# Kernel optimization log

Measured on AMD Instinct MI355X. Metric: run time of the kernel, lower is better.

Reference implementation:

```python
import jax, jax.numpy as jnp
import numpy as np

WS = 8        # window size
NH = 3        # num heads (head_dim = 192/3 = 64)
EPS = 1e-5    # BatchNorm eps


def conv1x1(x, w, b):
    # x: [B,C,H,W], w: [O,C], b: [O]  (1x1 conv == per-pixel matmul)
    return jnp.einsum('bchw,oc->bohw', x, w) + b[None, :, None, None]


def bn(x, gamma, beta, mean, var):
    # eval-mode BatchNorm2d
    scale = gamma / jnp.sqrt(var + EPS)
    return x * scale[None, :, None, None] + (beta - mean * scale)[None, :, None, None]


def window_partition_nchw(x, ws):
    # Faithful replication of the torch view/permute sequence (incl. its
    # channel/width interleaving inside each window).
    B, C, H, W = x.shape
    pad_h = (ws - H % ws) % ws
    pad_w = (ws - W % ws) % ws
    if pad_h or pad_w:
        x = jnp.pad(x, ((0, 0), (0, 0), (0, pad_h), (0, pad_w)))
    Hp, Wp = H + pad_h, W + pad_w
    x = x.reshape(B, C, Hp // ws, ws, Wp)
    windows = jnp.transpose(x, (0, 2, 4, 1, 3)).reshape(-1, C, ws, ws)
    return windows, (Hp, Wp)


def window_unpartition_nchw(windows, ws, pad_hw, hw):
    Hp, Wp = pad_hw
    H, W = hw
    B = windows.shape[0] // (Hp * Wp // ws // ws)
    C = windows.shape[1]
    x = windows.reshape(B, Hp // ws, Wp // ws, C, ws * ws)
    x = jnp.transpose(x, (0, 3, 1, 2, 4)).reshape(B, C, Hp, Wp)
    return x[:, :, :H, :W]


def attention(x, qkv_w, qkv_b, proj_w, proj_b):
    # x: [Nwin, C, ws, ws]
    B, C, H, W = x.shape
    qkv = conv1x1(x, qkv_w, qkv_b)              # [B, 3*D, H, W]
    D = qkv.shape[1] // 3
    hd = D // NH
    qkv = qkv.reshape(B, 3, NH, hd, H * W)
    q, k, v = qkv[:, 0], qkv[:, 1], qkv[:, 2]   # [B, NH, hd, N]
    scale = hd ** -0.5
    attn = jnp.einsum('bhdn,bhdm->bhnm', q, k) * scale   # [B,NH,Nq,Nk]
    attn = jax.nn.softmax(attn, axis=-1)
    o = jnp.einsum('bhdm,bhnm->bhdn', v, attn).reshape(B, D, H, W)
    return conv1x1(o, proj_w, proj_b)


def setup_inputs() -> dict:
    key = jax.random.key(0)
    ks = jax.random.split(key, 16)
    B, C, H, W = 16, 192, 128, 128
    D = C            # dim_out == dim
    HID = 4 * D      # mlp_ratio = 4
    s = 0.02
    inp = {
        'x':           jax.random.normal(ks[0], (B, C, H, W), jnp.float32),
        'bn1_gamma':   jnp.ones((C,), jnp.float32),
        'bn1_beta':    jnp.zeros((C,), jnp.float32),
        'bn1_mean':    jax.random.normal(ks[1], (C,), jnp.float32) * 0.1,
        'bn1_var':     jax.random.uniform(ks[2], (C,), jnp.float32, 0.5, 1.5),
        'qkv_w':       jax.random.normal(ks[3], (3 * D, C), jnp.float32) * s,
        'qkv_b':       jnp.zeros((3 * D,), jnp.float32),
        'attn_proj_w': jax.random.normal(ks[4], (D, D), jnp.float32) * s,
        'attn_proj_b': jnp.zeros((D,), jnp.float32),
        'bn2_gamma':   jnp.ones((D,), jnp.float32),
        'bn2_beta':    jnp.zeros((D,), jnp.float32),
        'bn2_mean':    jax.random.normal(ks[5], (D,), jnp.float32) * 0.1,
        'bn2_var':     jax.random.uniform(ks[6], (D,), jnp.float32, 0.5, 1.5),
        'mlp_w1':      jax.random.normal(ks[7], (HID, D), jnp.float32) * s,
        'mlp_b1':      jnp.zeros((HID,), jnp.float32),
        'mlp_w2':      jax.random.normal(ks[8], (D, HID), jnp.float32) * s,
        'mlp_b2':      jnp.zeros((D,), jnp.float32),
    }
    return inp


def reference(x, bn1_gamma, bn1_beta, bn1_mean, bn1_var,
              qkv_w, qkv_b, attn_proj_w, attn_proj_b,
              bn2_gamma, bn2_beta, bn2_mean, bn2_var,
              mlp_w1, mlp_b1, mlp_w2, mlp_b2):
    shortcut = x
    h = bn(x, bn1_gamma, bn1_beta, bn1_mean, bn1_var)
    win, pad_hw = window_partition_nchw(h, WS)
    a = attention(win, qkv_w, qkv_b, attn_proj_w, attn_proj_b)
    a = window_unpartition_nchw(a, WS, pad_hw, (x.shape[2], x.shape[3]))
    x2 = shortcut + a                       # residual 1 (drop_path = identity)
    m = bn(x2, bn2_gamma, bn2_beta, bn2_mean, bn2_var)
    m = conv1x1(m, mlp_w1, mlp_b1)
    m = jax.nn.gelu(m, approximate=False)   # torch nn.GELU default (exact erf)
    m = conv1x1(m, mlp_w2, mlp_b2)
    return x2 + m                           # residual 2
```

## Files before the change

### kernel.cpp

```cpp
#include <hip/hip_runtime.h>
#include <hip/hip_bf16.h>
#include <math.h>

#define DI __device__ __forceinline__

typedef short bf16x8 __attribute__((ext_vector_type(8)));
typedef float f32x4 __attribute__((ext_vector_type(4)));
typedef unsigned short u16;

DI u16 f2bf(float f){
  unsigned u = __float_as_uint(f);
  unsigned r = (u + 0x7FFFu + ((u>>16)&1u)) >> 16;
  return (u16)r;
}
DI float bf2f(u16 h){ return __uint_as_float(((unsigned)h)<<16); }
DI unsigned pack2(float a, float b){ return (unsigned)f2bf(a) | ((unsigned)f2bf(b)<<16); }
DI float gelu_exact(float v){ return 0.5f*v*(1.0f + erff(v*0.70710678118654752f)); }

DI void gload_lds16(const void* g, const void* l){
  __builtin_amdgcn_global_load_lds((const __attribute__((address_space(1))) void*)g,
                                   (__attribute__((address_space(3))) void*)(void*)l, 16, 0, 0);
}

__global__ __launch_bounds__(256) void k0_prep(const float* __restrict__ qkvw,
    const float* __restrict__ pw, const float* __restrict__ w1, const float* __restrict__ w2,
    u16* __restrict__ wq, u16* __restrict__ wp, u16* __restrict__ w1b, u16* __restrict__ w2b){
  int i = blockIdx.x*256 + threadIdx.x;
  if (i < 122880){
    int r = i/192;
    u16 v = 0;
    if (r < 576) v = f2bf(qkvw[i]);
    wq[i] = v;
  } else if (i < 172032){
    int j = i-122880; int r = j/192;
    u16 v = 0;
    if (r < 192) v = f2bf(pw[j]);
    wp[j] = v;
  } else if (i < 319488){
    int j = i-172032; w1b[j] = f2bf(w1[j]);
  } else if (i < 516096){
    int j = i-319488; int r = j/768;
    u16 v = 0;
    if (r < 192) v = f2bf(w2[j]);
    w2b[j] = v;
  }
}

__global__ __launch_bounds__(512) void k1_part(const float* __restrict__ x,
    const float* __restrict__ g1, const float* __restrict__ b1,
    const float* __restrict__ m1, const float* __restrict__ v1,
    u16* __restrict__ win_t){
  __shared__ u16 so[4*64*200];
  int tid = threadIdx.x;
  int bx = blockIdx.x;
  int wg = bx & 3, hb = (bx>>2)&15, b = bx>>6;
#pragma unroll
  for (int i=0;i<24;i++){
    int lin = i*512 + tid;
    int w4 = lin & 7;
    int rowid = lin >> 3;
    int c = rowid >> 3, jj = rowid & 7;
    float sc = g1[c]*rsqrtf(v1[c]+1e-5f);
    float sh = b1[c] - m1[c]*sc;
    float4 xv = *(const float4*)(x + (((size_t)(b*192 + c)*128 + hb*8 + jj)*128 + wg*32 + w4*4));
    int cg = c>>3, ci = c&7;
    int t = ci*8 + jj;
    float vv[4] = {xv.x, xv.y, xv.z, xv.w};
#pragma unroll
    for (int k=0;k<4;k++){
      int w = w4*4 + k;
      int wig = w>>3, q = w&7;
      so[(wig*64 + t)*200 + q*24 + cg] = f2bf(vv[k]*sc + sh);
    }
  }
  __syncthreads();
  int rowi = tid>>1, half = tid&1;
  size_t tok0 = ((size_t)((b*16+hb)*16 + wg*4))*64;
  u16* dst = win_t + (tok0 + rowi)*192 + half*96;
  const u16* src = so + rowi*200 + half*96;
#pragma unroll
  for (int ch=0; ch<12; ch++)
    *(uint4*)(dst + ch*8) = *(const uint4*)(src + ch*8);
}

template<int EPI>
__global__ __launch_bounds__(256) void gemm_k(
    const u16* __restrict__ A, const u16* __restrict__ B,
    const float* __restrict__ bias, const float* __restrict__ x2,
    u16* __restrict__ outA, u16* __restrict__ outB, float* __restrict__ outF,
    int K, int Mtiles, int Mvalid, size_t Nstr)
{
  __shared__ u16 As[128*32];
  __shared__ u16 Bs[128*32];
  int tid = threadIdx.x;
  int wid = tid>>6, lane = tid&63;
  int lm = lane&15, g = lane>>4;
  int bx = blockIdx.x;
  int mt = bx % Mtiles;
  size_t n0 = (size_t)(bx / Mtiles) * 128;
  int m0 = mt*128;
  int wm = wid>>1, wn = wid&1;

  f32x4 acc[4][4];
#pragma unroll
  for (int i=0;i<4;i++)
#pragma unroll
    for (int j=0;j<4;j++) acc[i][j] = (f32x4){0.f,0.f,0.f,0.f};

  int nK = K >> 5;
  for (int kt=0; kt<nK; kt++){
    int kk = kt<<5;
#pragma unroll
    for (int s=0;s<2;s++){
      int seg = s*256 + tid;
      int row = seg>>2, ch = seg&3;
      int chs = ch ^ (row&3);
      gload_lds16(A + (size_t)(m0+row)*K + kk + chs*8, (const char*)As + (s*256 + wid*64)*16);
      gload_lds16(B + (n0+(size_t)row)*K + kk + chs*8, (const char*)Bs + (s*256 + wid*64)*16);
    }
    asm volatile("s_waitcnt vmcnt(0)" ::: "memory");
    __syncthreads();
    bf16x8 af[4], bfr[4];
#pragma unroll
    for (int i=0;i<4;i++){
      int row = wm*64 + i*16 + lm;
      af[i]  = *(const bf16x8*)&As[row*32 + ((g ^ (row&3))<<3)];
      int rb  = wn*64 + i*16 + lm;
      bfr[i] = *(const bf16x8*)&Bs[rb*32 + ((g ^ (rb&3))<<3)];
    }
#pragma unroll
    for (int i=0;i<4;i++)
#pragma unroll
      for (int j=0;j<4;j++)
        acc[i][j] = __builtin_amdgcn_mfma_f32_16x16x32_bf16(af[i], bfr[j], acc[i][j], 0,0,0);
    __syncthreads();
  }

  int baseM = m0 + wm*64;
  size_t nbase = n0 + wn*64;

  if (EPI == 0){
    if (m0 < 384){
#pragma unroll
      for (int i=0;i<4;i++){
        int mcol = baseM + i*16 + 4*g;
        float b0=bias[mcol], b1_=bias[mcol+1], b2_=bias[mcol+2], b3_=bias[mcol+3];
#pragma unroll
        for (int j=0;j<4;j++){
          size_t tok = nbase + j*16 + lm;
          f32x4 v = acc[i][j];
          uint2 w; w.x = pack2(v[0]+b0, v[1]+b1_); w.y = pack2(v[2]+b2_, v[3]+b3_);
          *(uint2*)(outA + tok*384 + mcol) = w;
        }
      }
    } else {
#pragma unroll
      for (int i=0;i<4;i++)
#pragma unroll
        for (int j=0;j<4;j++){
          f32x4 v = acc[i][j];
#pragma unroll
          for (int r=0;r<4;r++){
            int m = baseM + i*16 + 4*g + r;
            if (m < Mvalid){
              size_t tok = nbase + j*16 + lm;
              outB[(size_t)(m-384)*Nstr + tok] = f2bf(v[r] + bias[m]);
            }
          }
        }
    }
  }
  if (EPI == 1){
#pragma unroll
    for (int i=0;i<4;i++)
#pragma unroll
      for (int j=0;j<4;j++){
        f32x4 v = acc[i][j];
#pragma unroll
        for (int r=0;r<4;r++){
          int m = baseM + i*16 + 4*g + r;
          if (m < Mvalid){
            size_t tok = nbase + j*16 + lm;
            outB[(size_t)m*Nstr + tok] = f2bf(v[r] + bias[m]);
          }
        }
      }
  }
  if (EPI == 2){
#pragma unroll
    for (int i=0;i<4;i++){
      int mcol = baseM + i*16 + 4*g;
      float b0=bias[mcol], b1_=bias[mcol+1], b2_=bias[mcol+2], b3_=bias[mcol+3];
#pragma unroll
      for (int j=0;j<4;j++){
        size_t tok = nbase + j*16 + lm;
        f32x4 v = acc[i][j];
        uint2 w;
        w.x = pack2(gelu_exact(v[0]+b0), gelu_exact(v[1]+b1_));
        w.y = pack2(gelu_exact(v[2]+b2_), gelu_exact(v[3]+b3_));
        *(uint2*)(outA + tok*768 + mcol) = w;
      }
    }
  }
  if (EPI == 3){
#pragma unroll
    for (int i=0;i<4;i++)
#pragma unroll
      for (int j=0;j<4;j++){
        f32x4 v = acc[i][j];
#pragma unroll
        for (int r=0;r<4;r++){
          int m = baseM + i*16 + 4*g + r;
          if (m < Mvalid){
            size_t nn = nbase + j*16 + lm;
            size_t bimg = nn>>14; size_t p = nn & 16383;
            size_t off = (bimg*192 + m)*16384 + p;
            outF[off] = v[r] + bias[m] + x2[off];
          }
        }
      }
  }
}

__global__ __launch_bounds__(192) void k3_attn(const u16* __restrict__ qkt,
    const u16* __restrict__ vb, u16* __restrict__ ot, size_t Nstr){
  __shared__ u16 lds[3*3*4096];
  int tid = threadIdx.x;
  int hd = tid>>6;
  int lane = tid&63;
  int lm = lane&15, g = lane>>4;
  size_t win = blockIdx.x;
  u16* Kt = lds + hd*3*4096;
  u16* Vt = Kt + 4096;
  u16* QP = Vt + 4096;
  size_t tokb = win*64;

#pragma unroll
  for (int it=0; it<8; it++){
    int seg = it*64 + lane;
    int row = seg>>3, c16 = seg&7;
    int cs = (c16 ^ (row&7))*8;
    gload_lds16(qkt + (tokb+row)*384 + 192 + hd*64 + cs, (const char*)Kt + it*1024);
    gload_lds16(qkt + (tokb+row)*384 +       hd*64 + cs, (const char*)QP + it*1024);
    gload_lds16(vb + (size_t)(hd*64+row)*Nstr + tokb + cs, (const char*)Vt + it*1024);
  }
  asm volatile("s_waitcnt vmcnt(0)" ::: "memory");

  bf16x8 ak[4][2];
#pragma unroll
  for (int mt2=0; mt2<4; mt2++)
#pragma unroll
    for (int kd=0; kd<2; kd++){
      int row = mt2*16 + lm;
      ak[mt2][kd] = *(const bf16x8*)&Kt[row*64 + (((kd*4+g) ^ (row&7))<<3)];
    }

  float rinv[4];
#pragma unroll
  for (int nt=0; nt<4; nt++){
    int rowq = nt*16 + lm;
    bf16x8 bq0 = *(const bf16x8*)&QP[rowq*64 + (((0+g) ^ (rowq&7))<<3)];
    bf16x8 bq1 = *(const bf16x8*)&QP[rowq*64 + (((4+g) ^ (rowq&7))<<3)];
    f32x4 sa[4];
#pragma unroll
    for (int mt2=0; mt2<4; mt2++){
      f32x4 z = (f32x4){0.f,0.f,0.f,0.f};
      z = __builtin_amdgcn_mfma_f32_16x16x32_bf16(ak[mt2][0], bq0, z, 0,0,0);
      z = __builtin_amdgcn_mfma_f32_16x16x32_bf16(ak[mt2][1], bq1, z, 0,0,0);
      sa[mt2] = z;
    }
    float mx = -1e30f;
#pragma unroll
    for (int mt2=0; mt2<4; mt2++)
#pragma unroll
      for (int r=0;r<4;r++) mx = fmaxf(mx, sa[mt2][r]);
    mx = fmaxf(mx, __shfl_xor(mx, 16));
    mx = fmaxf(mx, __shfl_xor(mx, 32));
    float sum = 0.f;
    float e[4][4];
#pragma unroll
    for (int mt2=0; mt2<4; mt2++)
#pragma unroll
      for (int r=0;r<4;r++){ float t = __expf(0.125f*(sa[mt2][r]-mx)); e[mt2][r] = t; sum += t; }
    sum += __shfl_xor(sum, 16);
    sum += __shfl_xor(sum, 32);
    rinv[nt] = 1.0f / sum;
    int n = nt*16 + lm;
#pragma unroll
    for (int mt2=0; mt2<4; mt2++)
#pragma unroll
      for (int pr=0; pr<2; pr++){
        int m = mt2*16 + 4*g + pr*2;
        *(unsigned*)&QP[n*64 + (((m>>3) ^ (n&7))<<3) + (m&7)] = pack2(e[mt2][pr*2], e[mt2][pr*2+1]);
      }
  }

  f32x4 oa[4][4];
#pragma unroll
  for (int i=0;i<4;i++)
#pragma unroll
    for (int j=0;j<4;j++) oa[i][j] = (f32x4){0.f,0.f,0.f,0.f};
  bf16x8 av[4][2];
#pragma unroll
  for (int dt=0; dt<4; dt++)
#pragma unroll
    for (int km=0; km<2; km++){
      int row = dt*16 + lm;
      av[dt][km] = *(const bf16x8*)&Vt[row*64 + (((km*4+g) ^ (row&7))<<3)];
    }
#pragma unroll
  for (int nt=0; nt<4; nt++){
    int rowp = nt*16 + lm;
    bf16x8 bp0 = *(const bf16x8*)&QP[rowp*64 + (((0+g) ^ (rowp&7))<<3)];
    bf16x8 bp1 = *(const bf16x8*)&QP[rowp*64 + (((4+g) ^ (rowp&7))<<3)];
#pragma unroll
    for (int dt=0; dt<4; dt++){
      oa[dt][nt] = __builtin_amdgcn_mfma_f32_16x16x32_bf16(av[dt][0], bp0, oa[dt][nt], 0,0,0);
      oa[dt][nt] = __builtin_amdgcn_mfma_f32_16x16x32_bf16(av[dt][1], bp1, oa[dt][nt], 0,0,0);
    }
  }
#pragma unroll
  for (int nt=0; nt<4; nt++){
    size_t tok = tokb + nt*16 + lm;
#pragma unroll
    for (int dt=0; dt<4; dt++){
      f32x4 v = oa[dt][nt];
      uint2 w;
      w.x = pack2(v[0]*rinv[nt], v[1]*rinv[nt]);
      w.y = pack2(v[2]*rinv[nt], v[3]*rinv[nt]);
      *(uint2*)(ot + tok*192 + hd*64 + dt*16 + 4*g) = w;
    }
  }
}

__global__ __launch_bounds__(512) void k5_unpart(const u16* __restrict__ aw,
    const float* __restrict__ x, float* __restrict__ x2, size_t Nstr){
  __shared__ u16 abuf[192*288];
  int tid = threadIdx.x;
  int bx = blockIdx.x;
  int wg = bx&3, hb = (bx>>2)&15, b = bx>>6;
  size_t tok0 = ((size_t)((b*16+hb)*16 + wg*4))*64;
#pragma unroll
  for (int i=0;i<12;i++){
    int idx = i*512 + tid;
    int cp = idx>>5, l32 = idx&31;
    uint4 v = *(const uint4*)(aw + (size_t)cp*Nstr + tok0 + l32*8);
    int q = cp/24, cg = cp - q*24;
    int ci = l32&7, wig = l32>>3;
    int c = cg*8 + ci;
    const u16* pv = (const u16*)&v;
#pragma unroll
    for (int k=0;k<8;k++)
      abuf[c*288 + k*36 + wig*8 + q] = pv[k];
  }
  __syncthreads();
#pragma unroll
  for (int i=0;i<24;i++){
    int lin = i*512 + tid;
    int w4 = lin&7, rowid = lin>>3;
    int c = rowid>>3, jj = rowid&7;
    size_t xoff = ((size_t)(b*192 + c)*128 + hb*8 + jj)*128 + wg*32 + w4*4;
    float4 xv = *(const float4*)(x + xoff);
    float vv[4] = {xv.x, xv.y, xv.z, xv.w};
    float4 o;
    o.x = vv[0] + bf2f(abuf[c*288 + jj*36 + w4*4 + 0]);
    o.y = vv[1] + bf2f(abuf[c*288 + jj*36 + w4*4 + 1]);
    o.z = vv[2] + bf2f(abuf[c*288 + jj*36 + w4*4 + 2]);
    o.w = vv[3] + bf2f(abuf[c*288 + jj*36 + w4*4 + 3]);
    *(float4*)(x2 + xoff) = o;
  }
}

__global__ __launch_bounds__(256) void k5b_t(const float* __restrict__ x2,
    const float* __restrict__ g2, const float* __restrict__ be2,
    const float* __restrict__ m2, const float* __restrict__ v2,
    u16* __restrict__ h2t){
  __shared__ u16 t[64*260];
  int tid = threadIdx.x;
  int bx = blockIdx.x;
  int b = bx/192; int rem = bx - b*192; int cb = rem>>6; int pb = rem&63;
#pragma unroll
  for (int i=0;i<16;i++){
    int idx = i*256 + tid;
    int cr = idx>>6, p4 = idx&63;
    int c = cb*64 + cr;
    float sc = g2[c]*rsqrtf(v2[c]+1e-5f);
    float sh = be2[c] - m2[c]*sc;
    float4 v = *(const float4*)(x2 + ((size_t)(b*192+c)*16384 + pb*256 + p4*4));
    uint2 w; w.x = pack2(v.x*sc+sh, v.y*sc+sh); w.y = pack2(v.z*sc+sh, v.w*sc+sh);
    *(uint2*)&t[cr*260 + p4*4] = w;
  }
  __syncthreads();
  size_t tokg = (size_t)b*16384 + pb*256 + tid;
  u16* dst = h2t + tokg*192 + cb*64;
#pragma unroll
  for (int cc=0; cc<8; cc++){
    u16 tmp[8];
#pragma unroll
    for (int k=0;k<8;k++) tmp[k] = t[(cc*8+k)*260 + tid];
    *(uint4*)(dst + cc*8) = *(const uint4*)tmp;
  }
}

extern "C" void kernel_launch(void* const* d_in, const int* in_sizes, int n_in,
                              void* d_out, int out_size, void* d_ws, size_t ws_size,
                              hipStream_t stream){
  const float* x   = (const float*)d_in[0];
  const float* g1  = (const float*)d_in[1];
  const float* be1 = (const float*)d_in[2];
  const float* mu1 = (const float*)d_in[3];
  const float* va1 = (const float*)d_in[4];
  const float* qkvw= (const float*)d_in[5];
  const float* qkvb= (const float*)d_in[6];
  const float* pw  = (const float*)d_in[7];
  const float* pb  = (const float*)d_in[8];
  const float* g2  = (const float*)d_in[9];
  const float* be2 = (const float*)d_in[10];
  const float* mu2 = (const float*)d_in[11];
  const float* va2 = (const float*)d_in[12];
  const float* w1  = (const float*)d_in[13];
  const float* b1  = (const float*)d_in[14];
  const float* w2  = (const float*)d_in[15];
  const float* b2  = (const float*)d_in[16];
  float* out = (float*)d_out;
  char* ws = (char*)d_ws;

  const size_t MB = 1048576;
  u16*  wint = (u16*) (ws + 0*MB);
  u16*  vbuf = (u16*) (ws + 24*MB);
  u16*  o_t  = (u16*) (ws + 48*MB);
  u16*  awin = (u16*) (ws + 72*MB);
  u16*  gt   = (u16*) (ws + 0*MB);
  u16*  qkt  = (u16*) (ws + 96*MB);
  u16*  h2t  = (u16*) (ws + 96*MB);
  u16*  wq   = (u16*) (ws + 144*MB);
  u16*  wp   = wq  + 640*192;
  u16*  w1b  = wp  + 256*192;
  u16*  w2b  = w1b + 768*192;
  const size_t needed = 144*MB + 1032192;
  if (ws_size < needed) return;

  const size_t SLICE_TOK = 65536;
  const size_t SLICE_ELT = SLICE_TOK * 192;

  k0_prep<<<2016,256,0,stream>>>(qkvw, pw, w1, w2, wq, wp, w1b, w2b);

  for (int s=0; s<4; s++){
    const float* xs = x   + (size_t)s*SLICE_ELT;
    float*      x2s = out + (size_t)s*SLICE_ELT;
    k1_part<<<256,512,0,stream>>>(xs, g1, be1, mu1, va1, wint);
    gemm_k<0><<<512*5,256,0,stream>>>(wq, wint, qkvb, nullptr,
                                      qkt, vbuf, nullptr, 192, 5, 576, SLICE_TOK);
    k3_attn<<<1024,192,0,stream>>>(qkt, vbuf, o_t, SLICE_TOK);
    gemm_k<1><<<512*2,256,0,stream>>>(wp, o_t, pb, nullptr,
                                      nullptr, awin, nullptr, 192, 2, 192, SLICE_TOK);
    k5_unpart<<<256,512,0,stream>>>(awin, xs, x2s, SLICE_TOK);
  }

  for (int s=0; s<4; s++){
    float* x2s = out + (size_t)s*SLICE_ELT;
    k5b_t<<<768,256,0,stream>>>(x2s, g2, be2, mu2, va2, h2t);
    gemm_k<2><<<512*6,256,0,stream>>>(w1b, h2t, b1, nullptr,
                                      gt, nullptr, nullptr, 192, 6, 768, SLICE_TOK);
    gemm_k<3><<<512*2,256,0,stream>>>(w2b, gt, b2, x2s,
                                      nullptr, nullptr, x2s, 768, 2, 192, SLICE_TOK);
  }
}
```

Measured before the change: 1.618 ms.

## Process all tokens in one pass, fuse BN2 transpose into unpartition, remap GEMM blocks

Drops the four-way token slicing, so each stage runs once over all 262144 tokens with larger grids. A much larger workspace holds the full-size intermediates. The BN2 plus transpose kernel is folded into the unpartition kernel, which now writes both x2 and the bf16 token-major normalized activations through a swizzled LDS buffer, avoiding a re-read of x2. GEMM block IDs are remapped across 8 groups (likely meant to match XCD dispatch) to improve cache locality. The trade-offs are higher workspace memory and more register pressure in the fused kernel (48 packed values per thread).

```diff
diff --git a/kernel.cpp b/kernel.cpp
--- a/kernel.cpp
+++ b/kernel.cpp
@@ -95,9 +95,12 @@
   int tid = threadIdx.x;
   int wid = tid>>6, lane = tid&63;
   int lm = lane&15, g = lane>>4;
-  int bx = blockIdx.x;
-  int mt = bx % Mtiles;
-  size_t n0 = (size_t)(bx / Mtiles) * 128;
+  int nwg = gridDim.x;
+  int chunk = nwg >> 3;
+  int bid = blockIdx.x;
+  int wgid = (bid & 7) * chunk + (bid >> 3);
+  int mt = wgid % Mtiles;
+  size_t n0 = (size_t)(wgid / Mtiles) * 128;
   int m0 = mt*128;
   int wm = wid>>1, wn = wid&1;
 
@@ -334,7 +337,10 @@
 }
 
 __global__ __launch_bounds__(512) void k5_unpart(const u16* __restrict__ aw,
-    const float* __restrict__ x, float* __restrict__ x2, size_t Nstr){
+    const float* __restrict__ x,
+    const float* __restrict__ g2, const float* __restrict__ be2,
+    const float* __restrict__ m2, const float* __restrict__ v2,
+    float* __restrict__ x2, u16* __restrict__ h2t, size_t Nstr){
   __shared__ u16 abuf[192*288];
   int tid = threadIdx.x;
   int bx = blockIdx.x;
@@ -354,51 +360,48 @@
       abuf[c*288 + k*36 + wig*8 + q] = pv[k];
   }
   __syncthreads();
+  unsigned hreg[48];
 #pragma unroll
   for (int i=0;i<24;i++){
     int lin = i*512 + tid;
     int w4 = lin&7, rowid = lin>>3;
     int c = rowid>>3, jj = rowid&7;
+    float sc = g2[c]*rsqrtf(v2[c]+1e-5f);
+    float sh = be2[c] - m2[c]*sc;
     size_t xoff = ((size_t)(b*192 + c)*128 + hb*8 + jj)*128 + wg*32 + w4*4;
     float4 xv = *(const float4*)(x + xoff);
-    float vv[4] = {xv.x, xv.y, xv.z, xv.w};
     float4 o;
-    o.x = vv[0] + bf2f(abuf[c*288 + jj*36 + w4*4 + 0]);
-    o.y = vv[1] + bf2f(abuf[c*288 + jj*36 + w4*4 + 1]);
-    o.z = vv[2] + bf2f(abuf[c*288 + jj*36 + w4*4 + 2]);
-    o.w = vv[3] + bf2f(abuf[c*288 + jj*36 + w4*4 + 3]);
+    o.x = xv.x + bf2f(abuf[c*288 + jj*36 + w4*4 + 0]);
+    o.y = xv.y + bf2f(abuf[c*288 + jj*36 + w4*4 + 1]);
+    o.z = xv.z + bf2f(abuf[c*288 + jj*36 + w4*4 + 2]);
+    o.w = xv.w + bf2f(abuf[c*288 + jj*36 + w4*4 + 3]);
     *(float4*)(x2 + xoff) = o;
-  }
-}
-
-__global__ __launch_bounds__(256) void k5b_t(const float* __restrict__ x2,
-    const float* __restrict__ g2, const float* __restrict__ be2,
-    const float* __restrict__ m2, const float* __restrict__ v2,
-    u16* __restrict__ h2t){
-  __shared__ u16 t[64*260];
-  int tid = threadIdx.x;
-  int bx = blockIdx.x;
-  int b = bx/192; int rem = bx - b*192; int cb = rem>>6; int pb = rem&63;
-#pragma unroll
-  for (int i=0;i<16;i++){
-    int idx = i*256 + tid;
-    int cr = idx>>6, p4 = idx&63;
-    int c = cb*64 + cr;
-    float sc = g2[c]*rsqrtf(v2[c]+1e-5f);
-    float sh = be2[c] - m2[c]*sc;
-    float4 v = *(const float4*)(x2 + ((size_t)(b*192+c)*16384 + pb*256 + p4*4));
-    uint2 w; w.x = pack2(v.x*sc+sh, v.y*sc+sh); w.y = pack2(v.z*sc+sh, v.w*sc+sh);
-    *(uint2*)&t[cr*260 + p4*4] = w;
+    hreg[i*2]   = pack2(o.x*sc+sh, o.y*sc+sh);
+    hreg[i*2+1] = pack2(o.z*sc+sh, o.w*sc+sh);
   }
   __syncthreads();
-  size_t tokg = (size_t)b*16384 + pb*256 + tid;
-  u16* dst = h2t + tokg*192 + cb*64;
-#pragma unroll
-  for (int cc=0; cc<8; cc++){
-    u16 tmp[8];
-#pragma unroll
-    for (int k=0;k<8;k++) tmp[k] = t[(cc*8+k)*260 + tid];
-    *(uint4*)(dst + cc*8) = *(const uint4*)tmp;
+#pragma unroll
+  for (int i=0;i<24;i++){
+    int lin = i*512 + tid;
+    int w4 = lin&7, rowid = lin>>3;
+    int c = rowid>>3, jj = rowid&7;
+    const u16* hv = (const u16*)&hreg[i*2];
+#pragma unroll
+    for (int k=0;k<4;k++){
+      int lt = jj*32 + w4*4 + k;
+      abuf[lt*192 + (c ^ ((lt&7)<<3))] = hv[k];
+    }
+  }
+  __syncthreads();
+  int rowi = tid>>1, half = tid&1;
+  int jj2 = rowi>>5, w2 = rowi&31;
+  size_t tokg = (size_t)b*16384 + (size_t)(hb*8 + jj2)*128 + wg*32 + w2;
+  u16* dst = h2t + tokg*192;
+#pragma unroll
+  for (int ch=0; ch<12; ch++){
+    int cc = half*12 + ch;
+    uint4 v = *(const uint4*)&abuf[rowi*192 + (((cc*16) ^ ((rowi&7)<<4))>>1)];
+    *(uint4*)(dst + cc*8) = v;
   }
 }
 
@@ -427,42 +430,31 @@
 
   const size_t MB = 1048576;
   u16*  wint = (u16*) (ws + 0*MB);
-  u16*  vbuf = (u16*) (ws + 24*MB);
-  u16*  o_t  = (u16*) (ws + 48*MB);
-  u16*  awin = (u16*) (ws + 72*MB);
-  u16*  gt   = (u16*) (ws + 0*MB);
+  u16*  o_t  = (u16*) (ws + 0*MB);
+  u16*  h2t  = (u16*) (ws + 0*MB);
   u16*  qkt  = (u16*) (ws + 96*MB);
-  u16*  h2t  = (u16*) (ws + 96*MB);
-  u16*  wq   = (u16*) (ws + 144*MB);
+  u16*  awin = (u16*) (ws + 96*MB);
+  u16*  gt   = (u16*) (ws + 96*MB);
+  u16*  vbuf = (u16*) (ws + 288*MB);
+  u16*  wq   = (u16*) (ws + 480*MB);
   u16*  wp   = wq  + 640*192;
   u16*  w1b  = wp  + 256*192;
   u16*  w2b  = w1b + 768*192;
-  const size_t needed = 144*MB + 1032192;
+  const size_t needed = 480*MB + 1032192;
   if (ws_size < needed) return;
 
-  const size_t SLICE_TOK = 65536;
-  const size_t SLICE_ELT = SLICE_TOK * 192;
+  const size_t NTOK = 262144;
 
   k0_prep<<<2016,256,0,stream>>>(qkvw, pw, w1, w2, wq, wp, w1b, w2b);
-
-  for (int s=0; s<4; s++){
-    const float* xs = x   + (size_t)s*SLICE_ELT;
-    float*      x2s = out + (size_t)s*SLICE_ELT;
-    k1_part<<<256,512,0,stream>>>(xs, g1, be1, mu1, va1, wint);
-    gemm_k<0><<<512*5,256,0,stream>>>(wq, wint, qkvb, nullptr,
-                                      qkt, vbuf, nullptr, 192, 5, 576, SLICE_TOK);
-    k3_attn<<<1024,192,0,stream>>>(qkt, vbuf, o_t, SLICE_TOK);
-    gemm_k<1><<<512*2,256,0,stream>>>(wp, o_t, pb, nullptr,
-                                      nullptr, awin, nullptr, 192, 2, 192, SLICE_TOK);
-    k5_unpart<<<256,512,0,stream>>>(awin, xs, x2s, SLICE_TOK);
-  }
-
-  for (int s=0; s<4; s++){
-    float* x2s = out + (size_t)s*SLICE_ELT;
-    k5b_t<<<768,256,0,stream>>>(x2s, g2, be2, mu2, va2, h2t);
-    gemm_k<2><<<512*6,256,0,stream>>>(w1b, h2t, b1, nullptr,
-                                      gt, nullptr, nullptr, 192, 6, 768, SLICE_TOK);
-    gemm_k<3><<<512*2,256,0,stream>>>(w2b, gt, b2, x2s,
-                                      nullptr, nullptr, x2s, 768, 2, 192, SLICE_TOK);
-  }
-}
+  k1_part<<<1024,512,0,stream>>>(x, g1, be1, mu1, va1, wint);
+  gemm_k<0><<<10240,256,0,stream>>>(wq, wint, qkvb, nullptr,
+                                    qkt, vbuf, nullptr, 192, 5, 576, NTOK);
+  k3_attn<<<4096,192,0,stream>>>(qkt, vbuf, o_t, NTOK);
+  gemm_k<1><<<4096,256,0,stream>>>(wp, o_t, pb, nullptr,
+                                   nullptr, awin, nullptr, 192, 2, 192, NTOK);
+  k5_unpart<<<1024,512,0,stream>>>(awin, x, g2, be2, mu2, va2, out, h2t, NTOK);
+  gemm_k<2><<<12288,256,0,stream>>>(w1b, h2t, b1, nullptr,
+                                    gt, nullptr, nullptr, 192, 6, 768, NTOK);
+  gemm_k<3><<<4096,256,0,stream>>>(w2b, gt, b2, out,
+                                   nullptr, nullptr, out, 768, 2, 192, NTOK);
+}
```

New measurement: 1.585 ms. 2.1% less time.
